# Kernel optimization log

Measured on AMD Instinct MI355X. Metric: run time of the kernel, lower is better.

The kernel has to match this reference:

```python
import jax, jax.numpy as jnp
import numpy as np

FACTOR = -1.0  # RecurrentAdditiveCell(units=11, factor=-1)


def setup_inputs() -> dict:
    key = jax.random.key(0)
    B, S, F = 1024, 4096, 11
    x = jax.random.normal(key, (B, S, F), dtype=jnp.float32)
    initial_state = jnp.zeros((B, 1), dtype=jnp.float32)
    return {"x": x, "initial_state": initial_state}


def reference(x, initial_state):
    # Cell: state_t = state_{t-1} + FACTOR * x_t, unrolled over time.
    # Equivalent closed form: init (broadcast over feat) + FACTOR * cumsum(x, time).
    # return_sequences=True -> emit every step's state: [B, S, F]
    y = initial_state[:, None, :] + FACTOR * jnp.cumsum(x, axis=1)
    return y
```

## Files before the change

### kernel.cpp

```cpp
#include <hip/hip_runtime.h>


#define BATCH    1024
#define SEQ      4096
#define FEAT     11
#define FACTOR   (-1.0f)

#define NTHREADS 256
#define TS       512
#define NT       (SEQ / TS)
#define CPT      (TS / NTHREADS)
#define TILE_FLOATS (TS * FEAT)
#define TILE_F4  (TILE_FLOATS / 4)
#define VLMAX    ((TILE_F4 + NTHREADS - 1) / NTHREADS)

__global__ __launch_bounds__(NTHREADS, 4)
void rnn_scan_kernel(const float* __restrict__ x,
                     const float* __restrict__ init_state,
                     float* __restrict__ y) {
    __shared__ float4 tile_lds[TILE_F4];
    __shared__ float  waveTot[4][FEAT];

    const int b    = blockIdx.x;
    const int t    = threadIdx.x;
    const int lane = t & 63;
    const int wav  = t >> 6;

    const float4* __restrict__ xg =
        (const float4*)(x + (size_t)b * (SEQ * FEAT));
    float4* __restrict__ yg =
        (float4*)(y + (size_t)b * (SEQ * FEAT));
    const float init_v = init_state[b];

    float carry[FEAT];
#pragma unroll
    for (int f = 0; f < FEAT; ++f) carry[f] = 0.0f;

    float4 cur[VLMAX];
#pragma unroll
    for (int i = 0; i < VLMAX; ++i) {
        int idx = t + NTHREADS * i;
        if (idx < TILE_F4) cur[i] = xg[idx];
    }

#pragma unroll
    for (int tile = 0; tile < NT; ++tile) {
#pragma unroll
        for (int i = 0; i < VLMAX; ++i) {
            int idx = t + NTHREADS * i;
            if (idx < TILE_F4) tile_lds[idx] = cur[i];
        }
        __syncthreads();

        if (tile + 1 < NT) {
#pragma unroll
            for (int i = 0; i < VLMAX; ++i) {
                int idx = t + NTHREADS * i;
                if (idx < TILE_F4) cur[i] = xg[(tile + 1) * TILE_F4 + idx];
            }
        }

        const float2* lds2 = (const float2*)tile_lds;
        float L[2 * FEAT];
#pragma unroll
        for (int m = 0; m < FEAT; ++m) {
            float2 q = lds2[FEAT * t + m];
            L[2 * m]     = q.x;
            L[2 * m + 1] = q.y;
        }
        float inc[FEAT];
#pragma unroll
        for (int f = 0; f < FEAT; ++f) {
            L[FEAT + f] += L[f];
            inc[f] = L[FEAT + f];
        }
#pragma unroll
        for (int d = 1; d < 64; d <<= 1) {
#pragma unroll
            for (int f = 0; f < FEAT; ++f) {
                float o = __shfl_up(inc[f], d, 64);
                if (lane >= d) inc[f] += o;
            }
        }
        if (lane == 63) {
#pragma unroll
            for (int f = 0; f < FEAT; ++f) waveTot[wav][f] = inc[f];
        }
        __syncthreads();

        float2* lds2w = (float2*)tile_lds;
#pragma unroll
        for (int f = 0; f < FEAT; ++f) {
            float off = carry[f] + inc[f] - L[FEAT + f];
#pragma unroll
            for (int w = 0; w < 4; ++w) {
                float wt = waveTot[w][f];
                if (w < wav) off += wt;
                carry[f] += wt;
            }
            L[f]        = init_v + FACTOR * (off + L[f]);
            L[FEAT + f] = init_v + FACTOR * (off + L[FEAT + f]);
        }
#pragma unroll
        for (int m = 0; m < FEAT; ++m)
            lds2w[FEAT * t + m] = make_float2(L[2 * m], L[2 * m + 1]);
        __syncthreads();

#pragma unroll
        for (int i = 0; i < VLMAX; ++i) {
            int idx = t + NTHREADS * i;
            if (idx < TILE_F4) yg[tile * TILE_F4 + idx] = tile_lds[idx];
        }
    }
}

extern "C" void kernel_launch(void* const* d_in, const int* in_sizes, int n_in,
                              void* d_out, int out_size, void* d_ws, size_t ws_size,
                              hipStream_t stream) {
    const float* x    = (const float*)d_in[0];
    const float* init = (const float*)d_in[1];
    float*       y    = (float*)d_out;
    rnn_scan_kernel<<<dim3(BATCH), dim3(NTHREADS), 0, stream>>>(x, init, y);
}
```

Before: 355.2 us.

## Split per-batch sequential scan into reduce-then-scan kernels over chunks

The single kernel, which ran one block per batch and walked the sequence tile by tile, becomes two kernels with one block per (batch, chunk). The first kernel computes per-chunk feature totals into workspace. The second kernel adds up the preceding chunk totals as an offset and scans its chunk locally. Wave scans now use DPP instead of shuffles, and tiles are loaded straight into LDS with global_load_lds. The aim is to fill the GPU with 8x more blocks and hide memory latency, at the cost of reading x twice plus a second launch.

```diff
diff --git a/kernel.cpp b/kernel.cpp
--- a/kernel.cpp
+++ b/kernel.cpp
@@ -8,109 +8,150 @@
 
 #define NTHREADS 256
 #define TS       512
-#define NT       (SEQ / TS)
-#define CPT      (TS / NTHREADS)
-#define TILE_FLOATS (TS * FEAT)
-#define TILE_F4  (TILE_FLOATS / 4)
-#define VLMAX    ((TILE_F4 + NTHREADS - 1) / NTHREADS)
+#define NC       (SEQ / TS)
+#define NBLK     (BATCH * NC)
+#define TILE_F4  (TS * FEAT / 4)
+#define VLMAX    6
+#define NWAVE    (NTHREADS / 64)
 
-__global__ __launch_bounds__(NTHREADS, 4)
-void rnn_scan_kernel(const float* __restrict__ x,
-                     const float* __restrict__ init_state,
-                     float* __restrict__ y) {
-    __shared__ float4 tile_lds[TILE_F4];
-    __shared__ float  waveTot[4][FEAT];
+template <int CTRL, int RM, int BM, bool BC>
+__device__ __forceinline__ float dpp_src(float v) {
+    int r = __builtin_amdgcn_update_dpp(0, __float_as_int(v), CTRL, RM, BM, BC);
+    return __int_as_float(r);
+}
 
-    const int b    = blockIdx.x;
+__device__ __forceinline__ float wave_iscan(float x) {
+    x += dpp_src<0x111, 0xf, 0xf, true >(x);
+    x += dpp_src<0x112, 0xf, 0xf, true >(x);
+    x += dpp_src<0x114, 0xf, 0xf, true >(x);
+    x += dpp_src<0x118, 0xf, 0xf, true >(x);
+    x += dpp_src<0x142, 0xa, 0xf, false>(x);
+    x += dpp_src<0x143, 0xc, 0xf, false>(x);
+    return x;
+}
+
+__device__ __forceinline__ void gload_lds16(const float4* g, float4* l) {
+    __builtin_amdgcn_global_load_lds(
+        (const __attribute__((address_space(1))) void*)g,
+        (__attribute__((address_space(3))) void*)l, 16, 0, 0);
+}
+
+__global__ __launch_bounds__(NTHREADS, 8)
+void partial_kernel(const float* __restrict__ x, float* __restrict__ partials) {
+    __shared__ float4 tile[TILE_F4];
+    __shared__ float  waveSum[NWAVE][FEAT];
+
+    const int blk  = blockIdx.x;
+    const int t    = threadIdx.x;
+    const int lane = t & 63;
+    const int wav  = t >> 6;
+    const float4* xg = (const float4*)x + (size_t)blk * TILE_F4;
+
+#pragma unroll
+    for (int i = 0; i < VLMAX; ++i) {
+        int idx = t + NTHREADS * i;
+        if (idx < TILE_F4) gload_lds16(xg + idx, &tile[idx]);
+    }
+    __syncthreads();
+
+    const float2* lds2 = (const float2*)tile;
+    float s[FEAT];
+#pragma unroll
+    for (int f = 0; f < FEAT; ++f) s[f] = 0.0f;
+#pragma unroll
+    for (int m = 0; m < FEAT; ++m) {
+        float2 q = lds2[FEAT * t + m];
+        s[(2 * m) % FEAT]     += q.x;
+        s[(2 * m + 1) % FEAT] += q.y;
+    }
+#pragma unroll
+    for (int f = 0; f < FEAT; ++f) s[f] = wave_iscan(s[f]);
+    if (lane == 63) {
+#pragma unroll
+        for (int f = 0; f < FEAT; ++f) waveSum[wav][f] = s[f];
+    }
+    __syncthreads();
+    if (t < FEAT) {
+        float p = waveSum[0][t] + waveSum[1][t] + waveSum[2][t] + waveSum[3][t];
+        partials[(size_t)blk * FEAT + t] = p;
+    }
+}
+
+__global__ __launch_bounds__(NTHREADS, 8)
+void scan_kernel(const float* __restrict__ x,
+                 const float* __restrict__ init_state,
+                 const float* __restrict__ partials,
+                 float* __restrict__ y) {
+    __shared__ float4 tile[TILE_F4];
+    __shared__ float  waveTot[NWAVE][FEAT];
+    __shared__ float  offsh[FEAT];
+
+    const int blk  = blockIdx.x;
+    const int b    = blk >> 3;
+    const int c    = blk & (NC - 1);
     const int t    = threadIdx.x;
     const int lane = t & 63;
     const int wav  = t >> 6;
 
-    const float4* __restrict__ xg =
-        (const float4*)(x + (size_t)b * (SEQ * FEAT));
-    float4* __restrict__ yg =
-        (float4*)(y + (size_t)b * (SEQ * FEAT));
+    const float4* xg = (const float4*)x + (size_t)blk * TILE_F4;
+    float4*       yg = (float4*)y + (size_t)blk * TILE_F4;
     const float init_v = init_state[b];
 
-    float carry[FEAT];
-#pragma unroll
-    for (int f = 0; f < FEAT; ++f) carry[f] = 0.0f;
-
-    float4 cur[VLMAX];
 #pragma unroll
     for (int i = 0; i < VLMAX; ++i) {
         int idx = t + NTHREADS * i;
-        if (idx < TILE_F4) cur[i] = xg[idx];
+        if (idx < TILE_F4) gload_lds16(xg + idx, &tile[idx]);
     }
+    if (t < FEAT) {
+        float o = 0.0f;
+#pragma unroll
+        for (int cc = 0; cc < NC - 1; ++cc) {
+            float pv = partials[(size_t)(b * NC + cc) * FEAT + t];
+            if (cc < c) o += pv;
+        }
+        offsh[t] = o;
+    }
+    __syncthreads();
+
+    const float2* lds2 = (const float2*)tile;
+    float L[2 * FEAT];
+#pragma unroll
+    for (int m = 0; m < FEAT; ++m) {
+        float2 q = lds2[FEAT * t + m];
+        L[2 * m]     = q.x;
+        L[2 * m + 1] = q.y;
+    }
+    float inc[FEAT];
+#pragma unroll
+    for (int f = 0; f < FEAT; ++f) {
+        L[FEAT + f] += L[f];
+        inc[f] = wave_iscan(L[FEAT + f]);
+    }
+    if (lane == 63) {
+#pragma unroll
+        for (int f = 0; f < FEAT; ++f) waveTot[wav][f] = inc[f];
+    }
+    __syncthreads();
+
+    float2* ldsw = (float2*)tile;
+#pragma unroll
+    for (int f = 0; f < FEAT; ++f) {
+        float off = offsh[f] + inc[f] - L[FEAT + f];
+#pragma unroll
+        for (int w = 0; w < NWAVE; ++w)
+            if (w < wav) off += waveTot[w][f];
+        L[f]        = init_v + FACTOR * (off + L[f]);
+        L[FEAT + f] = init_v + FACTOR * (off + L[FEAT + f]);
+    }
+#pragma unroll
+    for (int m = 0; m < FEAT; ++m)
+        ldsw[FEAT * t + m] = make_float2(L[2 * m], L[2 * m + 1]);
+    __syncthreads();
 
 #pragma unroll
-    for (int tile = 0; tile < NT; ++tile) {
-#pragma unroll
-        for (int i = 0; i < VLMAX; ++i) {
-            int idx = t + NTHREADS * i;
-            if (idx < TILE_F4) tile_lds[idx] = cur[i];
-        }
-        __syncthreads();
-
-        if (tile + 1 < NT) {
-#pragma unroll
-            for (int i = 0; i < VLMAX; ++i) {
-                int idx = t + NTHREADS * i;
-                if (idx < TILE_F4) cur[i] = xg[(tile + 1) * TILE_F4 + idx];
-            }
-        }
-
-        const float2* lds2 = (const float2*)tile_lds;
-        float L[2 * FEAT];
-#pragma unroll
-        for (int m = 0; m < FEAT; ++m) {
-            float2 q = lds2[FEAT * t + m];
-            L[2 * m]     = q.x;
-            L[2 * m + 1] = q.y;
-        }
-        float inc[FEAT];
-#pragma unroll
-        for (int f = 0; f < FEAT; ++f) {
-            L[FEAT + f] += L[f];
-            inc[f] = L[FEAT + f];
-        }
-#pragma unroll
-        for (int d = 1; d < 64; d <<= 1) {
-#pragma unroll
-            for (int f = 0; f < FEAT; ++f) {
-                float o = __shfl_up(inc[f], d, 64);
-                if (lane >= d) inc[f] += o;
-            }
-        }
-        if (lane == 63) {
-#pragma unroll
-            for (int f = 0; f < FEAT; ++f) waveTot[wav][f] = inc[f];
-        }
-        __syncthreads();
-
-        float2* lds2w = (float2*)tile_lds;
-#pragma unroll
-        for (int f = 0; f < FEAT; ++f) {
-            float off = carry[f] + inc[f] - L[FEAT + f];
-#pragma unroll
-            for (int w = 0; w < 4; ++w) {
-                float wt = waveTot[w][f];
-                if (w < wav) off += wt;
-                carry[f] += wt;
-            }
-            L[f]        = init_v + FACTOR * (off + L[f]);
-            L[FEAT + f] = init_v + FACTOR * (off + L[FEAT + f]);
-        }
-#pragma unroll
-        for (int m = 0; m < FEAT; ++m)
-            lds2w[FEAT * t + m] = make_float2(L[2 * m], L[2 * m + 1]);
-        __syncthreads();
-
-#pragma unroll
-        for (int i = 0; i < VLMAX; ++i) {
-            int idx = t + NTHREADS * i;
-            if (idx < TILE_F4) yg[tile * TILE_F4 + idx] = tile_lds[idx];
-        }
+    for (int i = 0; i < VLMAX; ++i) {
+        int idx = t + NTHREADS * i;
+        if (idx < TILE_F4) yg[idx] = tile[idx];
     }
 }
 
@@ -120,5 +161,7 @@
     const float* x    = (const float*)d_in[0];
     const float* init = (const float*)d_in[1];
     float*       y    = (float*)d_out;
-    rnn_scan_kernel<<<dim3(BATCH), dim3(NTHREADS), 0, stream>>>(x, init, y);
+    float*       part = (float*)d_ws;
+    partial_kernel<<<dim3(NBLK), dim3(NTHREADS), 0, stream>>>(x, part);
+    scan_kernel<<<dim3(NBLK), dim3(NTHREADS), 0, stream>>>(x, init, part, y);
 }
```

New measurement: 346.1 us. 2.6% less time.
